# Kernel optimization log

Measured on AMD Instinct MI355X. Metric: run time of the kernel, lower is better.

Reference implementation:

```python
import jax, jax.numpy as jnp
import numpy as np
from jax import lax

B, T, D, H, O, L = 128, 2048, 64, 128, 32, 2


def _rnn_layer(x, lengths, W_ih, W_hh, b_ih, b_hh):
    """One tanh RNN layer over padded [B,T,*] input with packed semantics:
    hidden state is frozen at steps t >= lengths[b] (those steps do not exist
    in the packed sequence). Returns per-step hidden states [B,T,H]."""
    Bl, Tl, _ = x.shape
    Hl = W_hh.shape[0]
    # precompute input projection once: [B,T,H]
    x_proj = jnp.einsum('btd,hd->bth', x, W_ih) + b_ih + b_hh

    def step(h, inp):
        xp, t = inp  # xp: [B,H], t: scalar
        h_new = jnp.tanh(xp + h @ W_hh.T)
        h = jnp.where((t < lengths)[:, None], h_new, h)
        return h, h

    h0 = jnp.zeros((Bl, Hl), dtype=x.dtype)
    _, ys = lax.scan(step, h0, (x_proj.transpose(1, 0, 2), jnp.arange(Tl)))
    return ys.transpose(1, 0, 2)  # [B,T,H]


def setup_inputs() -> dict:
    key = jax.random.key(0)
    ks = jax.random.split(key, 12)
    x = jax.random.normal(ks[0], (B, T, D), dtype=jnp.float32)
    # descending-sorted lengths in [1, T] (pack_padded_sequence enforce_sorted)
    lengths = jnp.sort(jax.random.randint(ks[1], (B,), 1, T + 1).astype(jnp.int32))[::-1]
    s_in = 1.0 / np.sqrt(H)
    W_ih0 = jax.random.uniform(ks[2], (H, D), minval=-s_in, maxval=s_in)
    W_hh0 = jax.random.uniform(ks[3], (H, H), minval=-s_in, maxval=s_in)
    b_ih0 = jax.random.uniform(ks[4], (H,), minval=-s_in, maxval=s_in)
    b_hh0 = jax.random.uniform(ks[5], (H,), minval=-s_in, maxval=s_in)
    W_ih1 = jax.random.uniform(ks[6], (H, H), minval=-s_in, maxval=s_in)
    W_hh1 = jax.random.uniform(ks[7], (H, H), minval=-s_in, maxval=s_in)
    b_ih1 = jax.random.uniform(ks[8], (H,), minval=-s_in, maxval=s_in)
    b_hh1 = jax.random.uniform(ks[9], (H,), minval=-s_in, maxval=s_in)
    W_fc = jax.random.uniform(ks[10], (O, H), minval=-s_in, maxval=s_in)
    b_fc = jax.random.uniform(ks[11], (O,), minval=-s_in, maxval=s_in)
    return {"x": x, "lengths": lengths,
            "W_ih0": W_ih0, "W_hh0": W_hh0, "b_ih0": b_ih0, "b_hh0": b_hh0,
            "W_ih1": W_ih1, "W_hh1": W_hh1, "b_ih1": b_ih1, "b_hh1": b_hh1,
            "W_fc": W_fc, "b_fc": b_fc}


def reference(x, lengths, W_ih0, W_hh0, b_ih0, b_hh0,
              W_ih1, W_hh1, b_ih1, b_hh1, W_fc, b_fc):
    h1 = _rnn_layer(x, lengths, W_ih0, W_hh0, b_ih0, b_hh0)   # [B,T,H]
    h2 = _rnn_layer(h1, lengths, W_ih1, W_hh1, b_ih1, b_hh1)  # [B,T,H]
    # pad_packed_sequence zero-fills positions t >= length
    mask = (jnp.arange(T)[None, :] < lengths[:, None])[..., None]
    out = jnp.where(mask, h2, 0.0)
    # fc is applied to the zero-padded tensor (padded rows become b_fc)
    return jnp.einsum('bth,oh->bto', out, W_fc) + b_fc
```

## Files before the change

kernel.cpp:

```cpp
#include <hip/hip_runtime.h>

#define BB 128
#define TT 2048
#define DD 64
#define HH 128
#define OO 32
#define NB 16
#define SCALE 2.885390081777927f

typedef _Float16 f16x8 __attribute__((ext_vector_type(8)));
typedef __fp16   pk16x2 __attribute__((ext_vector_type(2)));
typedef float    f32x4 __attribute__((ext_vector_type(4)));

#define MFMA16(a,b,c) __builtin_amdgcn_mfma_f32_16x16x32_f16((a),(b),(c),0,0,0)

__device__ __forceinline__ f32x4 load4(const float* p){ return *(const f32x4*)p; }

union U8 { uint2 u[2]; f16x8 v; };

__device__ __forceinline__ f16x8 afrag_s(const float* p, float s){
    float4 a = *(const float4*)p, b = *(const float4*)(p+4);
    f16x8 r;
    r[0]=(_Float16)(a.x*s); r[1]=(_Float16)(a.y*s); r[2]=(_Float16)(a.z*s); r[3]=(_Float16)(a.w*s);
    r[4]=(_Float16)(b.x*s); r[5]=(_Float16)(b.y*s); r[6]=(_Float16)(b.z*s); r[7]=(_Float16)(b.w*s);
    return r;
}

__device__ __forceinline__ float tanh_pre(float z){
#if __has_builtin(__builtin_amdgcn_exp2f)
    float e = __builtin_amdgcn_exp2f(z);
#else
    float e = exp2f(z);
#endif
    return __builtin_fmaf(-2.f, __builtin_amdgcn_rcpf(1.f + e), 1.f);
}

__device__ __forceinline__ unsigned pk2(float a, float b){
    union { pk16x2 h; unsigned u; } c;
    c.h = __builtin_amdgcn_cvt_pkrtz(a, b);
    return c.u;
}

__device__ __forceinline__ f16x8 xfrag(float4 a, float4 b){
    union { unsigned u[4]; f16x8 v; } c;
    c.u[0] = pk2(a.x, a.y); c.u[1] = pk2(a.z, a.w);
    c.u[2] = pk2(b.x, b.y); c.u[3] = pk2(b.z, b.w);
    return c.v;
}

#define LSTR2 132
#define PHB   (NB*LSTR2*2)

#define STEP_L1(T_, P_, XS_) do {                                             \
    const int t_ = (T_);                                                      \
    U8 bh1[4];                                                                \
    _Pragma("unroll")                                                         \
    for (int kt = 0; kt < 4; ++kt){                                           \
        bh1[kt].u[0] = *(const uint2*)(h1b + (P_)*PHB + kt*64);               \
        bh1[kt].u[1] = *(const uint2*)(h1b + (P_)*PHB + kt*64 + 8);           \
    }                                                                         \
    f32x4 z[2];                                                               \
    const bool doZ0 = (t_ < maxlen);                                          \
    if (doZ0){                                                                \
        f16x8 xB0 = xfrag(XS_[0], XS_[1]);                                    \
        f16x8 xB1 = xfrag(XS_[2], XS_[3]);                                    \
        _Pragma("unroll")                                                     \
        for (int m = 0; m < 2; ++m){                                          \
            z[m] = bv0[m];                                                    \
            z[m] = MFMA16(Aih[m][0], xB0, z[m]);                              \
            z[m] = MFMA16(Aih[m][1], xB1, z[m]);                              \
        }                                                                     \
        _Pragma("unroll")                                                     \
        for (int kt = 0; kt < 4; ++kt)                                        \
            _Pragma("unroll")                                                 \
            for (int m = 0; m < 2; ++m)                                       \
                z[m] = MFMA16(A0[m][kt], bh1[kt].v, z[m]);                    \
    }                                                                         \
    {           \
        const int tl = (t_ + 2 < TT) ? (t_ + 2) : (TT - 1);                   \
        const float* xq = xb + (size_t)tl*DD;                                 \
        XS_[0] = *(const float4*)(xq);                                        \
        XS_[1] = *(const float4*)(xq + 4);                                    \
        XS_[2] = *(const float4*)(xq + 32);                                   \
        XS_[3] = *(const float4*)(xq + 36);                                   \
    }                                                                         \
    if (doZ0){                                                                \
        _Pragma("unroll")                                                     \
        for (int m = 0; m < 2; ++m){                                          \
            uint2 v;                                                          \
            v.x = pk2(tanh_pre(z[m][0]), tanh_pre(z[m][1]));                  \
            v.y = pk2(tanh_pre(z[m][2]), tanh_pre(z[m][3]));                  \
            *(uint2*)((char*)H1T + ((P_)^1)*PHB + n*264 + (w*2+m)*32 + q*8) = v; \
        }                                                                     \
    }                                                                         \
    asm volatile("s_waitcnt lgkmcnt(0)\n\ts_barrier" ::: "memory");           \
} while (0)

#define STEP_L2(T_, P_) do {                                                  \
    const int t_ = (T_);                                                      \
    U8 bh1[4], bh2[4];                                                        \
    _Pragma("unroll")                                                         \
    for (int kt = 0; kt < 4; ++kt){                                           \
        bh1[kt].u[0] = *(const uint2*)(h1b + (P_)*PHB + kt*64);               \
        bh1[kt].u[1] = *(const uint2*)(h1b + (P_)*PHB + kt*64 + 8);           \
        bh2[kt].u[0] = *(const uint2*)(h2b + (P_)*PHB + kt*64);               \
        bh2[kt].u[1] = *(const uint2*)(h2b + (P_)*PHB + kt*64 + 8);           \
    }                                                                         \
    const bool doZ1 = (t_ >= 1) && (t_ <= maxlen);                            \
    f32x4 z[2];                                                               \
    if (doZ1){                                                                \
        f32x4 y[2];                                                           \
        _Pragma("unroll")                                                     \
        for (int m = 0; m < 2; ++m){                                          \
            z[m] = b1v[m];                                                    \
            y[m][0]=0.f; y[m][1]=0.f; y[m][2]=0.f; y[m][3]=0.f;               \
        }                                                                     \
        _Pragma("unroll")                                                     \
        for (int kt = 0; kt < 4; ++kt)                                        \
            _Pragma("unroll")                                                 \
            for (int m = 0; m < 2; ++m){                                      \
                z[m] = MFMA16(Ai[m][kt], bh1[kt].v, z[m]);                    \
                y[m] = MFMA16(Ah[m][kt], bh2[kt].v, y[m]);                    \
            }                                                                 \
        _Pragma("unroll")                                                     \
        for (int m = 0; m < 2; ++m) z[m] += y[m];                             \
    }                                                                         \
    if (doFC && t_ >= 2){                                                     \
        f32x4 zf = bfv;                                                       \
        _Pragma("unroll")                                                     \
        for (int kt = 0; kt < 4; ++kt) zf = MFMA16(Af[kt], bh2[kt].v, zf);    \
        if (t_ - 2 < lenn){                                                   \
            float4 sv; sv.x=zf[0]; sv.y=zf[1]; sv.z=zf[2]; sv.w=zf[3];        \
            *(float4*)(obase + (size_t)(t_-2)*OO) = sv;                       \
        }                                                                     \
    }                                                                         \
    if (doZ1){                                                                \
        _Pragma("unroll")                                                     \
        for (int m = 0; m < 2; ++m){                                          \
            uint2 v;                                                          \
            v.x = pk2(tanh_pre(z[m][0]), tanh_pre(z[m][1]));                  \
            v.y = pk2(tanh_pre(z[m][2]), tanh_pre(z[m][3]));                  \
            *(uint2*)((char*)H2T + ((P_)^1)*PHB + n*264 + (wl*2+m)*32 + q*8) = v; \
        }                                                                     \
    }                                                                         \
    asm volatile("s_waitcnt lgkmcnt(0)\n\ts_barrier" ::: "memory");           \
} while (0)

extern "C" __global__ void __launch_bounds__(512, 1)
scan_kernel(const float* __restrict__ x, const int* __restrict__ lengths,
            const float* __restrict__ W_ih0, const float* __restrict__ W_hh0,
            const float* __restrict__ b_ih0, const float* __restrict__ b_hh0,
            const float* __restrict__ W_ih1, const float* __restrict__ W_hh1,
            const float* __restrict__ b_ih1, const float* __restrict__ b_hh1,
            const float* __restrict__ W_fc,  const float* __restrict__ b_fc,
            float* __restrict__ out)
{
    const int tid  = threadIdx.x;
    const int w    = tid >> 6, lane = tid & 63;
    const int n    = lane & 15, q = lane >> 4;
    const int rbase= blockIdx.x * NB;

    __shared__ __align__(16) _Float16 H1T[2][NB][LSTR2];
    __shared__ __align__(16) _Float16 H2T[2][NB][LSTR2];

    for (int idx = tid; idx < (2*NB*LSTR2)/2; idx += 512){
        ((unsigned*)H1T)[idx] = 0u;
        ((unsigned*)H2T)[idx] = 0u;
    }

    const int lenn = lengths[rbase + n];
    int mx = lenn;
    #pragma unroll
    for (int s = 1; s < 16; s <<= 1){ int o = __shfl_xor(mx, s, 64); mx = max(mx, o); }
    const int maxlen = __builtin_amdgcn_readfirstlane(mx);

    const char* h1b = (const char*)H1T + n*264 + q*16;
    const char* h2b = (const char*)H2T + n*264 + q*16;

    __syncthreads();

    if (w < 4){
        f16x8 A0[2][4], Aih[2][2];
        f32x4 bv0[2];
        #pragma unroll
        for (int m = 0; m < 2; ++m){
            const int row = (w*2 + m)*16 + n;
            #pragma unroll
            for (int kt = 0; kt < 4; ++kt)
                A0[m][kt] = afrag_s(W_hh0 + row*HH + kt*32 + q*8, SCALE);
            #pragma unroll
            for (int kt = 0; kt < 2; ++kt)
                Aih[m][kt] = afrag_s(W_ih0 + row*DD + kt*32 + q*8, SCALE);
            bv0[m] = (load4(b_ih0 + (w*2+m)*16 + q*4)
                    + load4(b_hh0 + (w*2+m)*16 + q*4)) * SCALE;
        }

        const float* xb = x + ((size_t)(rbase+n)*TT)*DD + q*8;

        float4 xe[4], xo[4];
        {
            const float* x0 = xb;
            const float* x1 = xb + DD;
            xe[0] = *(const float4*)(x0);      xe[1] = *(const float4*)(x0 + 4);
            xe[2] = *(const float4*)(x0 + 32); xe[3] = *(const float4*)(x0 + 36);
            xo[0] = *(const float4*)(x1);      xo[1] = *(const float4*)(x1 + 4);
            xo[2] = *(const float4*)(x1 + 32); xo[3] = *(const float4*)(x1 + 36);
        }

        for (int t0 = 0; t0 <= maxlen + 1; t0 += 2){
            STEP_L1(t0,     0, xe);
            STEP_L1(t0 + 1, 1, xo);
        }
    } else {
        const int wl = w - 4;
        const bool doFC = (wl < 2);
        const int f = wl & 1;
        f16x8 Ai[2][4], Ah[2][4];
        f32x4 b1v[2];
        #pragma unroll
        for (int m = 0; m < 2; ++m){
            const int row = (wl*2 + m)*16 + n;
            #pragma unroll
            for (int kt = 0; kt < 4; ++kt){
                Ai[m][kt] = afrag_s(W_ih1 + row*HH + kt*32 + q*8, SCALE);
                Ah[m][kt] = afrag_s(W_hh1 + row*HH + kt*32 + q*8, SCALE);
            }
            b1v[m] = (load4(b_ih1 + (wl*2+m)*16 + q*4)
                    + load4(b_hh1 + (wl*2+m)*16 + q*4)) * SCALE;
        }
        f16x8 Af[4];
        #pragma unroll
        for (int kt = 0; kt < 4; ++kt)
            Af[kt] = afrag_s(W_fc + (f*16 + n)*HH + kt*32 + q*8, 1.0f);
        const f32x4 bfv = load4(b_fc + f*16 + q*4);

        float* obase = out + ((size_t)(rbase+n)*TT)*OO + f*16 + q*4;

        for (int t0 = 0; t0 <= maxlen + 1; t0 += 2){
            STEP_L2(t0,     0);
            STEP_L2(t0 + 1, 1);
        }
    }

    {
        const int row  = tid >> 5;
        const int lr   = lengths[rbase + row];
        const int o4   = tid & 7;
        const int tpar = (tid >> 3) & 3;
        const float4 bf4 = *(const float4*)(b_fc + o4*4);
        float* ob = out + ((size_t)(rbase+row)*TT)*OO + o4*4;
        for (int t = lr + tpar; t < TT; t += 4)
            *(float4*)(ob + (size_t)t*OO) = bf4;
    }
}

extern "C" void kernel_launch(void* const* d_in, const int* in_sizes, int n_in,
                              void* d_out, int out_size, void* d_ws, size_t ws_size,
                              hipStream_t stream)
{
    const float* x       = (const float*)d_in[0];
    const int*   lengths = (const int*)  d_in[1];
    const float* W_ih0   = (const float*)d_in[2];
    const float* W_hh0   = (const float*)d_in[3];
    const float* b_ih0   = (const float*)d_in[4];
    const float* b_hh0   = (const float*)d_in[5];
    const float* W_ih1   = (const float*)d_in[6];
    const float* W_hh1   = (const float*)d_in[7];
    const float* b_ih1   = (const float*)d_in[8];
    const float* b_hh1   = (const float*)d_in[9];
    const float* W_fc    = (const float*)d_in[10];
    const float* b_fc    = (const float*)d_in[11];

    scan_kernel<<<BB/NB, 512, 0, stream>>>(x, lengths, W_ih0, W_hh0,
                                           b_ih0, b_hh0,
                                           W_ih1, W_hh1, b_ih1, b_hh1,
                                           W_fc, b_fc, (float*)d_out);
}
```

Before: 1.592 ms.

## Split MFMA accumulator chains, widen LDS loads, and raise priority in RNN step

Splits each serial MFMA accumulation chain into two independent accumulators that are summed before the tanh, so dependent MFMAs can overlap on the recurrence critical path. Pads the LDS hidden-state row stride from 132 to 136 halves so each lane reads its fragment with a single 16-byte load instead of two 8-byte loads. Raises wave priority around the layer-2 MFMA block. The split adds extra adds and registers and changes the fp32 summation order slightly.

Result: no change. 1.584 ms (-0.5%).

```diff
diff --git a/kernel.cpp b/kernel.cpp
--- a/kernel.cpp
+++ b/kernel.cpp
@@ -16,8 +16,6 @@
 
 __device__ __forceinline__ f32x4 load4(const float* p){ return *(const f32x4*)p; }
 
-union U8 { uint2 u[2]; f16x8 v; };
-
 __device__ __forceinline__ f16x8 afrag_s(const float* p, float s){
     float4 a = *(const float4*)p, b = *(const float4*)(p+4);
     f16x8 r;
@@ -48,33 +46,34 @@
     return c.v;
 }
 
-#define LSTR2 132
+#define LSTR2 136
 #define PHB   (NB*LSTR2*2)
 
 #define STEP_L1(T_, P_, XS_) do {                                             \
     const int t_ = (T_);                                                      \
-    U8 bh1[4];                                                                \
+    f16x8 bh1[4];                                                             \
     _Pragma("unroll")                                                         \
-    for (int kt = 0; kt < 4; ++kt){                                           \
-        bh1[kt].u[0] = *(const uint2*)(h1b + (P_)*PHB + kt*64);               \
-        bh1[kt].u[1] = *(const uint2*)(h1b + (P_)*PHB + kt*64 + 8);           \
-    }                                                                         \
-    f32x4 z[2];                                                               \
+    for (int kt = 0; kt < 4; ++kt)                                            \
+        bh1[kt] = *(const f16x8*)(h1b + (P_)*PHB + kt*64);                    \
     const bool doZ0 = (t_ < maxlen);                                          \
+    f32x4 za[2], zb[2];                                                       \
     if (doZ0){                                                                \
         f16x8 xB0 = xfrag(XS_[0], XS_[1]);                                    \
         f16x8 xB1 = xfrag(XS_[2], XS_[3]);                                    \
         _Pragma("unroll")                                                     \
         for (int m = 0; m < 2; ++m){                                          \
-            z[m] = bv0[m];                                                    \
-            z[m] = MFMA16(Aih[m][0], xB0, z[m]);                              \
-            z[m] = MFMA16(Aih[m][1], xB1, z[m]);                              \
-        }                                                                     \
-        _Pragma("unroll")                                                     \
-        for (int kt = 0; kt < 4; ++kt)                                        \
-            _Pragma("unroll")                                                 \
-            for (int m = 0; m < 2; ++m)                                       \
-                z[m] = MFMA16(A0[m][kt], bh1[kt].v, z[m]);                    \
+            za[m] = bv0[m];                                                   \
+            za[m] = MFMA16(Aih[m][0], xB0, za[m]);                            \
+            zb[m][0]=0.f; zb[m][1]=0.f; zb[m][2]=0.f; zb[m][3]=0.f;           \
+            zb[m] = MFMA16(Aih[m][1], xB1, zb[m]);                            \
+        }                                                                     \
+        _Pragma("unroll")                                                     \
+        for (int m = 0; m < 2; ++m){                                          \
+            za[m] = MFMA16(A0[m][0], bh1[0], za[m]);                          \
+            zb[m] = MFMA16(A0[m][1], bh1[1], zb[m]);                          \
+            za[m] = MFMA16(A0[m][2], bh1[2], za[m]);                          \
+            zb[m] = MFMA16(A0[m][3], bh1[3], zb[m]);                          \
+        }                                                                     \
     }                                                                         \
     {           \
         const int tl = (t_ + 2 < TT) ? (t_ + 2) : (TT - 1);                   \
@@ -87,10 +86,11 @@
     if (doZ0){                                                                \
         _Pragma("unroll")                                                     \
         for (int m = 0; m < 2; ++m){                                          \
+            f32x4 zz = za[m] + zb[m];                                         \
             uint2 v;                                                          \
-            v.x = pk2(tanh_pre(z[m][0]), tanh_pre(z[m][1]));                  \
-            v.y = pk2(tanh_pre(z[m][2]), tanh_pre(z[m][3]));                  \
-            *(uint2*)((char*)H1T + ((P_)^1)*PHB + n*264 + (w*2+m)*32 + q*8) = v; \
+            v.x = pk2(tanh_pre(zz[0]), tanh_pre(zz[1]));                      \
+            v.y = pk2(tanh_pre(zz[2]), tanh_pre(zz[3]));                      \
+            *(uint2*)((char*)H1T + ((P_)^1)*PHB + n*272 + (w*2+m)*32 + q*8) = v; \
         }                                                                     \
     }                                                                         \
     asm volatile("s_waitcnt lgkmcnt(0)\n\ts_barrier" ::: "memory");           \
@@ -98,49 +98,56 @@
 
 #define STEP_L2(T_, P_) do {                                                  \
     const int t_ = (T_);                                                      \
-    U8 bh1[4], bh2[4];                                                        \
+    f16x8 bh1[4], bh2[4];                                                     \
     _Pragma("unroll")                                                         \
     for (int kt = 0; kt < 4; ++kt){                                           \
-        bh1[kt].u[0] = *(const uint2*)(h1b + (P_)*PHB + kt*64);               \
-        bh1[kt].u[1] = *(const uint2*)(h1b + (P_)*PHB + kt*64 + 8);           \
-        bh2[kt].u[0] = *(const uint2*)(h2b + (P_)*PHB + kt*64);               \
-        bh2[kt].u[1] = *(const uint2*)(h2b + (P_)*PHB + kt*64 + 8);           \
+        bh1[kt] = *(const f16x8*)(h1b + (P_)*PHB + kt*64);                    \
+        bh2[kt] = *(const f16x8*)(h2b + (P_)*PHB + kt*64);                    \
     }                                                                         \
     const bool doZ1 = (t_ >= 1) && (t_ <= maxlen);                            \
-    f32x4 z[2];                                                               \
+    f32x4 za[2], zb[2], ya[2], yb[2];                                         \
+    __builtin_amdgcn_s_setprio(1);                                            \
     if (doZ1){                                                                \
-        f32x4 y[2];                                                           \
-        _Pragma("unroll")                                                     \
-        for (int m = 0; m < 2; ++m){                                          \
-            z[m] = b1v[m];                                                    \
-            y[m][0]=0.f; y[m][1]=0.f; y[m][2]=0.f; y[m][3]=0.f;               \
-        }                                                                     \
-        _Pragma("unroll")                                                     \
-        for (int kt = 0; kt < 4; ++kt)                                        \
-            _Pragma("unroll")                                                 \
-            for (int m = 0; m < 2; ++m){                                      \
-                z[m] = MFMA16(Ai[m][kt], bh1[kt].v, z[m]);                    \
-                y[m] = MFMA16(Ah[m][kt], bh2[kt].v, y[m]);                    \
-            }                                                                 \
-        _Pragma("unroll")                                                     \
-        for (int m = 0; m < 2; ++m) z[m] += y[m];                             \
+        _Pragma("unroll")                                                     \
+        for (int m = 0; m < 2; ++m){                                          \
+            za[m] = b1v[m];                                                   \
+            zb[m][0]=0.f; zb[m][1]=0.f; zb[m][2]=0.f; zb[m][3]=0.f;           \
+            ya[m] = zb[m]; yb[m] = zb[m];                                     \
+        }                                                                     \
+        _Pragma("unroll")                                                     \
+        for (int m = 0; m < 2; ++m){                                          \
+            za[m] = MFMA16(Ai[m][0], bh1[0], za[m]);                          \
+            zb[m] = MFMA16(Ai[m][1], bh1[1], zb[m]);                          \
+            ya[m] = MFMA16(Ah[m][0], bh2[0], ya[m]);                          \
+            yb[m] = MFMA16(Ah[m][1], bh2[1], yb[m]);                          \
+            za[m] = MFMA16(Ai[m][2], bh1[2], za[m]);                          \
+            zb[m] = MFMA16(Ai[m][3], bh1[3], zb[m]);                          \
+            ya[m] = MFMA16(Ah[m][2], bh2[2], ya[m]);                          \
+            yb[m] = MFMA16(Ah[m][3], bh2[3], yb[m]);                          \
+        }                                                                     \
     }                                                                         \
     if (doFC && t_ >= 2){                                                     \
-        f32x4 zf = bfv;                                                       \
-        _Pragma("unroll")                                                     \
-        for (int kt = 0; kt < 4; ++kt) zf = MFMA16(Af[kt], bh2[kt].v, zf);    \
+        f32x4 zfa = bfv, zfb;                                                 \
+        zfb[0]=0.f; zfb[1]=0.f; zfb[2]=0.f; zfb[3]=0.f;                       \
+        zfa = MFMA16(Af[0], bh2[0], zfa);                                     \
+        zfb = MFMA16(Af[1], bh2[1], zfb);                                     \
+        zfa = MFMA16(Af[2], bh2[2], zfa);                                     \
+        zfb = MFMA16(Af[3], bh2[3], zfb);                                     \
         if (t_ - 2 < lenn){                                                   \
+            f32x4 zf = zfa + zfb;                                             \
             float4 sv; sv.x=zf[0]; sv.y=zf[1]; sv.z=zf[2]; sv.w=zf[3];        \
             *(float4*)(obase + (size_t)(t_-2)*OO) = sv;                       \
         }                                                                     \
     }                                                                         \
+    __builtin_amdgcn_s_setprio(0);                                            \
     if (doZ1){                                                                \
         _Pragma("unroll")                                                     \
         for (int m = 0; m < 2; ++m){                                          \
+            f32x4 zz = (za[m] + zb[m]) + (ya[m] + yb[m]);                     \
             uint2 v;                                                          \
-            v.x = pk2(tanh_pre(z[m][0]), tanh_pre(z[m][1]));                  \
-            v.y = pk2(tanh_pre(z[m][2]), tanh_pre(z[m][3]));                  \
-            *(uint2*)((char*)H2T + ((P_)^1)*PHB + n*264 + (wl*2+m)*32 + q*8) = v; \
+            v.x = pk2(tanh_pre(zz[0]), tanh_pre(zz[1]));                      \
+            v.y = pk2(tanh_pre(zz[2]), tanh_pre(zz[3]));                      \
+            *(uint2*)((char*)H2T + ((P_)^1)*PHB + n*272 + (wl*2+m)*32 + q*8) = v; \
         }                                                                     \
     }                                                                         \
     asm volatile("s_waitcnt lgkmcnt(0)\n\ts_barrier" ::: "memory");           \
@@ -174,8 +181,8 @@
     for (int s = 1; s < 16; s <<= 1){ int o = __shfl_xor(mx, s, 64); mx = max(mx, o); }
     const int maxlen = __builtin_amdgcn_readfirstlane(mx);
 
-    const char* h1b = (const char*)H1T + n*264 + q*16;
-    const char* h2b = (const char*)H2T + n*264 + q*16;
+    const char* h1b = (const char*)H1T + n*272 + q*16;
+    const char* h2b = (const char*)H2T + n*272 + q*16;
 
     __syncthreads();
 
```

## Replace block barriers with LDS progress flags and decouple layer pipelines

Applied to the files above, without the earlier changes.

Drops the per-step block-wide s_barrier in favour of per-wave progress counters in shared memory that waves poll with s_sleep. Layer-1 waves can now run up to a few steps ahead of layer-2 waves, so layer-1 state gets a 4-deep ring buffer while layer-2 keeps double buffering. It also widens the LDS row stride to 136 halves so each fragment is read with one 16-byte load. The price is spin-wait polling overhead and reliance on LDS memory ordering for correctness.

Result: slower. 2.223 ms (+39.6%).

```diff
diff --git a/kernel.cpp b/kernel.cpp
--- a/kernel.cpp
+++ b/kernel.cpp
@@ -16,8 +16,6 @@
 
 __device__ __forceinline__ f32x4 load4(const float* p){ return *(const f32x4*)p; }
 
-union U8 { uint2 u[2]; f16x8 v; };
-
 __device__ __forceinline__ f16x8 afrag_s(const float* p, float s){
     float4 a = *(const float4*)p, b = *(const float4*)(p+4);
     f16x8 r;
@@ -48,35 +46,44 @@
     return c.v;
 }
 
-#define LSTR2 132
+__device__ __forceinline__ void wait2(const volatile int* f, int n1, int n2){
+    for(;;){
+        int a0=f[0], a1=f[1], a2=f[2], a3=f[3];
+        int b0=f[4], b1=f[5], b2=f[6], b3=f[7];
+        int ma = min(min(a0,a1), min(a2,a3));
+        int mb = min(min(b0,b1), min(b2,b3));
+        if (ma >= n1 && mb >= n2) break;
+        __builtin_amdgcn_s_sleep(1);
+    }
+    asm volatile("" ::: "memory");
+}
+
+#define LSTR2 136
 #define PHB   (NB*LSTR2*2)
 
-#define STEP_L1(T_, P_, XS_) do {                                             \
+#define L1STEP(T_, XS_) do {                                                  \
     const int t_ = (T_);                                                      \
-    U8 bh1[4];                                                                \
+    wait2(PF, t_ - 1, t_ - 3);                                                \
+    const char* rp = (const char*)H1R + ((t_+3)&3)*PHB + n*272 + q*16;        \
+    f16x8 bh1[4];                                                             \
     _Pragma("unroll")                                                         \
-    for (int kt = 0; kt < 4; ++kt){                                           \
-        bh1[kt].u[0] = *(const uint2*)(h1b + (P_)*PHB + kt*64);               \
-        bh1[kt].u[1] = *(const uint2*)(h1b + (P_)*PHB + kt*64 + 8);           \
+    for (int kt = 0; kt < 4; ++kt)                                            \
+        bh1[kt] = *(const f16x8*)(rp + kt*64);                                \
+    f16x8 xB0 = xfrag(XS_[0], XS_[1]);                                        \
+    f16x8 xB1 = xfrag(XS_[2], XS_[3]);                                        \
+    f32x4 z[2];                                                               \
+    _Pragma("unroll")                                                         \
+    for (int m = 0; m < 2; ++m){                                              \
+        z[m] = bv0[m];                                                        \
+        z[m] = MFMA16(Aih[m][0], xB0, z[m]);                                  \
+        z[m] = MFMA16(Aih[m][1], xB1, z[m]);                                  \
     }                                                                         \
-    f32x4 z[2];                                                               \
-    const bool doZ0 = (t_ < maxlen);                                          \
-    if (doZ0){                                                                \
-        f16x8 xB0 = xfrag(XS_[0], XS_[1]);                                    \
-        f16x8 xB1 = xfrag(XS_[2], XS_[3]);                                    \
+    _Pragma("unroll")                                                         \
+    for (int kt = 0; kt < 4; ++kt)                                            \
         _Pragma("unroll")                                                     \
-        for (int m = 0; m < 2; ++m){                                          \
-            z[m] = bv0[m];                                                    \
-            z[m] = MFMA16(Aih[m][0], xB0, z[m]);                              \
-            z[m] = MFMA16(Aih[m][1], xB1, z[m]);                              \
-        }                                                                     \
-        _Pragma("unroll")                                                     \
-        for (int kt = 0; kt < 4; ++kt)                                        \
-            _Pragma("unroll")                                                 \
-            for (int m = 0; m < 2; ++m)                                       \
-                z[m] = MFMA16(A0[m][kt], bh1[kt].v, z[m]);                    \
-    }                                                                         \
-    {           \
+        for (int m = 0; m < 2; ++m)                                           \
+            z[m] = MFMA16(A0[m][kt], bh1[kt], z[m]);                          \
+    {             \
         const int tl = (t_ + 2 < TT) ? (t_ + 2) : (TT - 1);                   \
         const float* xq = xb + (size_t)tl*DD;                                 \
         XS_[0] = *(const float4*)(xq);                                        \
@@ -84,66 +91,17 @@
         XS_[2] = *(const float4*)(xq + 32);                                   \
         XS_[3] = *(const float4*)(xq + 36);                                   \
     }                                                                         \
-    if (doZ0){                                                                \
+    {   char* wp = (char*)H1R + (t_&3)*PHB + n*272 + (w*2)*32 + q*8;          \
         _Pragma("unroll")                                                     \
         for (int m = 0; m < 2; ++m){                                          \
             uint2 v;                                                          \
             v.x = pk2(tanh_pre(z[m][0]), tanh_pre(z[m][1]));                  \
             v.y = pk2(tanh_pre(z[m][2]), tanh_pre(z[m][3]));                  \
-            *(uint2*)((char*)H1T + ((P_)^1)*PHB + n*264 + (w*2+m)*32 + q*8) = v; \
+            *(uint2*)(wp + m*32) = v;                                         \
         }                                                                     \
     }                                                                         \
-    asm volatile("s_waitcnt lgkmcnt(0)\n\ts_barrier" ::: "memory");           \
-} while (0)
-
-#define STEP_L2(T_, P_) do {                                                  \
-    const int t_ = (T_);                                                      \
-    U8 bh1[4], bh2[4];                                                        \
-    _Pragma("unroll")                                                         \
-    for (int kt = 0; kt < 4; ++kt){                                           \
-        bh1[kt].u[0] = *(const uint2*)(h1b + (P_)*PHB + kt*64);               \
-        bh1[kt].u[1] = *(const uint2*)(h1b + (P_)*PHB + kt*64 + 8);           \
-        bh2[kt].u[0] = *(const uint2*)(h2b + (P_)*PHB + kt*64);               \
-        bh2[kt].u[1] = *(const uint2*)(h2b + (P_)*PHB + kt*64 + 8);           \
-    }                                                                         \
-    const bool doZ1 = (t_ >= 1) && (t_ <= maxlen);                            \
-    f32x4 z[2];                                                               \
-    if (doZ1){                                                                \
-        f32x4 y[2];                                                           \
-        _Pragma("unroll")                                                     \
-        for (int m = 0; m < 2; ++m){                                          \
-            z[m] = b1v[m];                                                    \
-            y[m][0]=0.f; y[m][1]=0.f; y[m][2]=0.f; y[m][3]=0.f;               \
-        }                                                                     \
-        _Pragma("unroll")                                                     \
-        for (int kt = 0; kt < 4; ++kt)                                        \
-            _Pragma("unroll")                                                 \
-            for (int m = 0; m < 2; ++m){                                      \
-                z[m] = MFMA16(Ai[m][kt], bh1[kt].v, z[m]);                    \
-                y[m] = MFMA16(Ah[m][kt], bh2[kt].v, y[m]);                    \
-            }                                                                 \
-        _Pragma("unroll")                                                     \
-        for (int m = 0; m < 2; ++m) z[m] += y[m];                             \
-    }                                                                         \
-    if (doFC && t_ >= 2){                                                     \
-        f32x4 zf = bfv;                                                       \
-        _Pragma("unroll")                                                     \
-        for (int kt = 0; kt < 4; ++kt) zf = MFMA16(Af[kt], bh2[kt].v, zf);    \
-        if (t_ - 2 < lenn){                                                   \
-            float4 sv; sv.x=zf[0]; sv.y=zf[1]; sv.z=zf[2]; sv.w=zf[3];        \
-            *(float4*)(obase + (size_t)(t_-2)*OO) = sv;                       \
-        }                                                                     \
-    }                                                                         \
-    if (doZ1){                                                                \
-        _Pragma("unroll")                                                     \
-        for (int m = 0; m < 2; ++m){                                          \
-            uint2 v;                                                          \
-            v.x = pk2(tanh_pre(z[m][0]), tanh_pre(z[m][1]));                  \
-            v.y = pk2(tanh_pre(z[m][2]), tanh_pre(z[m][3]));                  \
-            *(uint2*)((char*)H2T + ((P_)^1)*PHB + n*264 + (wl*2+m)*32 + q*8) = v; \
-        }                                                                     \
-    }                                                                         \
-    asm volatile("s_waitcnt lgkmcnt(0)\n\ts_barrier" ::: "memory");           \
+    asm volatile("s_waitcnt lgkmcnt(0)" ::: "memory");                        \
+    if (lane == 0) ((volatile int*)PF)[w] = t_;                               \
 } while (0)
 
 extern "C" __global__ void __launch_bounds__(512, 1)
@@ -160,22 +118,21 @@
     const int n    = lane & 15, q = lane >> 4;
     const int rbase= blockIdx.x * NB;
 
-    __shared__ __align__(16) _Float16 H1T[2][NB][LSTR2];
-    __shared__ __align__(16) _Float16 H2T[2][NB][LSTR2];
-
-    for (int idx = tid; idx < (2*NB*LSTR2)/2; idx += 512){
-        ((unsigned*)H1T)[idx] = 0u;
-        ((unsigned*)H2T)[idx] = 0u;
-    }
+    __shared__ __align__(16) _Float16 H1R[4][NB][LSTR2];
+    __shared__ __align__(16) _Float16 H2P[2][NB][LSTR2];
+    __shared__ int PF[8];
+
+    for (int idx = tid; idx < (6*NB*LSTR2)/2; idx += 512){
+        if (idx < (4*NB*LSTR2)/2) ((unsigned*)H1R)[idx] = 0u;
+        else ((unsigned*)H2P)[idx - (4*NB*LSTR2)/2] = 0u;
+    }
+    if (tid < 8) PF[tid] = -1;
 
     const int lenn = lengths[rbase + n];
     int mx = lenn;
     #pragma unroll
     for (int s = 1; s < 16; s <<= 1){ int o = __shfl_xor(mx, s, 64); mx = max(mx, o); }
     const int maxlen = __builtin_amdgcn_readfirstlane(mx);
-
-    const char* h1b = (const char*)H1T + n*264 + q*16;
-    const char* h2b = (const char*)H2T + n*264 + q*16;
 
     __syncthreads();
 
@@ -207,9 +164,9 @@
             xo[2] = *(const float4*)(x1 + 32); xo[3] = *(const float4*)(x1 + 36);
         }
 
-        for (int t0 = 0; t0 <= maxlen + 1; t0 += 2){
-            STEP_L1(t0,     0, xe);
-            STEP_L1(t0 + 1, 1, xo);
+        for (int t0 = 0; t0 < maxlen; t0 += 2){
+            L1STEP(t0, xe);
+            if (t0 + 1 < maxlen) L1STEP(t0 + 1, xo);
         }
     } else {
         const int wl = w - 4;
@@ -236,9 +193,59 @@
 
         float* obase = out + ((size_t)(rbase+n)*TT)*OO + f*16 + q*4;
 
-        for (int t0 = 0; t0 <= maxlen + 1; t0 += 2){
-            STEP_L2(t0,     0);
-            STEP_L2(t0 + 1, 1);
+        for (int u = 0; u <= maxlen; ++u){
+            const bool doRec = (u < maxlen);
+            const int n1 = doRec ? u : (maxlen - 1);
+            wait2(PF, n1, u - 1);
+            const char* rp2 = (const char*)H2P + ((u+1)&1)*PHB + n*272 + q*16;
+            f16x8 bh2[4];
+            #pragma unroll
+            for (int kt = 0; kt < 4; ++kt)
+                bh2[kt] = *(const f16x8*)(rp2 + kt*64);
+            f32x4 z[2];
+            if (doRec){
+                const char* rp1 = (const char*)H1R + (u&3)*PHB + n*272 + q*16;
+                f16x8 bh1[4];
+                #pragma unroll
+                for (int kt = 0; kt < 4; ++kt)
+                    bh1[kt] = *(const f16x8*)(rp1 + kt*64);
+                f32x4 y[2];
+                #pragma unroll
+                for (int m = 0; m < 2; ++m){
+                    z[m] = b1v[m];
+                    y[m][0]=0.f; y[m][1]=0.f; y[m][2]=0.f; y[m][3]=0.f;
+                }
+                #pragma unroll
+                for (int kt = 0; kt < 4; ++kt)
+                    #pragma unroll
+                    for (int m = 0; m < 2; ++m){
+                        z[m] = MFMA16(Ai[m][kt], bh1[kt], z[m]);
+                        y[m] = MFMA16(Ah[m][kt], bh2[kt], y[m]);
+                    }
+                #pragma unroll
+                for (int m = 0; m < 2; ++m) z[m] += y[m];
+            }
+            if (doFC && u >= 1){
+                f32x4 zf = bfv;
+                #pragma unroll
+                for (int kt = 0; kt < 4; ++kt) zf = MFMA16(Af[kt], bh2[kt], zf);
+                if (u - 1 < lenn){
+                    float4 sv; sv.x=zf[0]; sv.y=zf[1]; sv.z=zf[2]; sv.w=zf[3];
+                    *(float4*)(obase + (size_t)(u-1)*OO) = sv;
+                }
+            }
+            if (doRec){
+                char* wp = (char*)H2P + (u&1)*PHB + n*272 + (wl*2)*32 + q*8;
+                #pragma unroll
+                for (int m = 0; m < 2; ++m){
+                    uint2 v;
+                    v.x = pk2(tanh_pre(z[m][0]), tanh_pre(z[m][1]));
+                    v.y = pk2(tanh_pre(z[m][2]), tanh_pre(z[m][3]));
+                    *(uint2*)(wp + m*32) = v;
+                }
+            }
+            asm volatile("s_waitcnt lgkmcnt(0)" ::: "memory");
+            if (lane == 0) ((volatile int*)PF)[4 + wl] = u;
         }
     }
 
```
